# Kernel tuning notes

Hardware: AMD Instinct MI355X
Metric: run time of the kernel (lower is better)

## Reference

```python
import jax, jax.numpy as jnp
import numpy as np

N, J, H, O, SD = 6144, 2000, 100, 6144, 2


def setup_inputs() -> dict:
    key = jax.random.key(0)
    ks = jax.random.split(key, 18)
    sc = lambda fan_in: 1.0 / np.sqrt(fan_in)
    inp = {
        "gene_expr": jax.random.normal(ks[0], (N, J), jnp.float32),
        "spatial_pos": jax.random.normal(ks[1], (N, SD), jnp.float32),
        # linear weights stored [in, out] (y = x @ W + b)
        "Wq": jax.random.normal(ks[2], (J, H), jnp.float32) * sc(J),
        "bq": jnp.zeros((H,), jnp.float32),
        "Wk": jax.random.normal(ks[3], (J, H), jnp.float32) * sc(J),
        "bk": jnp.zeros((H,), jnp.float32),
        "Wv": jax.random.normal(ks[4], (J, O), jnp.float32) * sc(J),
        "bv": jnp.zeros((O,), jnp.float32),
        "Ws": jax.random.normal(ks[5], (SD, H), jnp.float32) * sc(SD),
        "bs": jnp.zeros((H,), jnp.float32),
        "W1": jax.random.normal(ks[6], (H, H), jnp.float32) * sc(H),
        "b1": jnp.zeros((H,), jnp.float32),
        "W2": jax.random.normal(ks[7], (H, H), jnp.float32) * sc(H),
        "b2": jnp.zeros((H,), jnp.float32),
        "Wf": jax.random.normal(ks[8], (H, 1), jnp.float32) * sc(H),
        "bf": jnp.zeros((1,), jnp.float32),
    }
    return inp


def reference(gene_expr, spatial_pos, Wq, bq, Wk, bk, Wv, bv, Ws, bs,
              W1, b1, W2, b2, Wf, bf):
    dk = jnp.sqrt(jnp.asarray(H, gene_expr.dtype))

    Q = gene_expr @ Wq + bq            # [N,H]
    K = gene_expr @ Wk + bk            # [N,H]
    V = gene_expr @ Wv + bv            # [N,O]

    # advanced spatial scalar + pairwise tanh difference
    sp = spatial_pos @ Ws + bs                             # [N,H]
    enh = jax.nn.relu(jnp.tanh(sp @ W1 + b1) @ W2 + b2)    # [N,H]
    f = (enh @ Wf + bf)[:, 0]                              # [N]
    fdiff = jnp.tanh(f[:, None] - f[None, :])              # [N,N]

    # gaussian kernel of squared pairwise distances (cdist p=2, sigma=1)
    sq = jnp.sum(spatial_pos * spatial_pos, axis=1)
    d2 = jnp.maximum(sq[:, None] + sq[None, :] - 2.0 * (spatial_pos @ spatial_pos.T), 0.0)
    spatial_sim = jnp.exp(-d2 / 2.0)                       # [N,N]

    # row-wise cosine similarity of gene expression
    norm = jnp.linalg.norm(gene_expr, axis=1, keepdims=True)
    xn = gene_expr / jnp.maximum(norm, 1e-12)
    cos_sim = xn @ xn.T                                    # [N,N]

    logits = (Q @ K.T) / dk + spatial_sim + cos_sim + fdiff
    attn = jax.nn.softmax(logits, axis=-1)                 # stable softmax == max-subtract in src
    out = attn @ V                                         # [N,O]
    return attn, out
```

## Files before the change

### kernel.cpp

```cpp
#include <hip/hip_runtime.h>
#include <stdint.h>
#include <math.h>

#define NN 6144
#define JJ 2000
#define HH 100
#define KB 2176
#define XOFF 128
#define KQK 2048

typedef __bf16 bf16;
typedef __bf16 bf16x8 __attribute__((ext_vector_type(8)));
typedef float f32x4 __attribute__((ext_vector_type(4)));

__device__ __forceinline__ void load_lds16(const void* g, void* l) {
  __builtin_amdgcn_global_load_lds(
      (const __attribute__((address_space(1))) void*)(uintptr_t)g,
      (__attribute__((address_space(3))) void*)(uint32_t)(uintptr_t)l,
      16, 0, 0);
}

template <int MODE>
__global__ __launch_bounds__(256, 2) void gemm_bt(
    const bf16* __restrict__ A, const bf16* __restrict__ B,
    int lda, int ldb, int kdim,
    const float* __restrict__ p0, const float* __restrict__ p1,
    const float* __restrict__ p2,
    bf16* __restrict__ ob0, bf16* __restrict__ ob1,
    float* __restrict__ of0, float* __restrict__ rowsum)
{
  __shared__ alignas(16) bf16 As[128 * 64];
  __shared__ alignas(16) bf16 Bs[128 * 64];

  const int tid = threadIdx.x;
  const int lane = tid & 63;
  const int wv = tid >> 6;
  const int m0 = blockIdx.x * 128;
  const int n0 = blockIdx.y * 128;

  const int srow = lane >> 3;
  const int scol = ((lane & 7) ^ srow) * 8;
  const bf16* gA = A + (size_t)(m0 + wv * 32 + srow) * lda + scol;
  const bf16* gB = B + (size_t)(n0 + wv * 32 + srow) * ldb + scol;
  bf16* lA0 = &As[(wv * 32) * 64];
  bf16* lB0 = &Bs[(wv * 32) * 64];

  const int l15 = lane & 15;
  const int l4 = lane >> 4;
  const int s7 = l15 & 7;
  const int wm = (wv >> 1) * 64;
  const int wn = (wv & 1) * 64;
  const bf16* ra0 = &As[(wm + l15) * 64 + ((l4 ^ s7) * 8)];
  const bf16* ra1 = &As[(wm + l15) * 64 + (((l4 + 4) ^ s7) * 8)];
  const bf16* rb0 = &Bs[(wn + l15) * 64 + ((l4 ^ s7) * 8)];
  const bf16* rb1 = &Bs[(wn + l15) * 64 + (((l4 + 4) ^ s7) * 8)];

  f32x4 acc[4][4];
#pragma unroll
  for (int i = 0; i < 4; ++i)
#pragma unroll
    for (int j = 0; j < 4; ++j) acc[i][j] = {0.f, 0.f, 0.f, 0.f};

  const int kiters = kdim >> 6;
  for (int kt = 0; kt < kiters; ++kt) {
    __syncthreads();
#pragma unroll
    for (int it = 0; it < 4; ++it) {
      load_lds16(gA + (size_t)it * 8 * lda, lA0 + it * 512);
      load_lds16(gB + (size_t)it * 8 * ldb, lB0 + it * 512);
    }
    gA += 64;
    gB += 64;
    __syncthreads();
#pragma unroll
    for (int ks = 0; ks < 2; ++ks) {
      const bf16* ra = ks ? ra1 : ra0;
      const bf16* rb = ks ? rb1 : rb0;
      bf16x8 af[4], bb[4];
#pragma unroll
      for (int i = 0; i < 4; ++i)
        af[i] = *(const bf16x8*)(ra + i * 1024);
#pragma unroll
      for (int j = 0; j < 4; ++j)
        bb[j] = *(const bf16x8*)(rb + j * 1024);
#pragma unroll
      for (int i = 0; i < 4; ++i)
#pragma unroll
        for (int j = 0; j < 4; ++j)
          acc[i][j] = __builtin_amdgcn_mfma_f32_16x16x32_bf16(af[i], bb[j], acc[i][j], 0, 0, 0);
    }
  }

  const int row_base = m0 + wm + l4 * 4;
  const int col_base = n0 + wn + l15;

  if (MODE == 3) {
#pragma unroll
    for (int i = 0; i < 4; ++i) {
#pragma unroll
      for (int r = 0; r < 4; ++r) {
        int row = row_base + i * 16 + r;
        float nm = p0[row];
#pragma unroll
        for (int j = 0; j < 4; ++j) {
          int h = col_base + j * 16;
          float v = acc[i][j][r] * nm;
          if (h < HH) ob0[(size_t)row * KB + h] = (bf16)((v + p1[h]) * 0.1f);
          else if (h < 2 * HH) ob1[(size_t)row * KB + (h - HH)] = (bf16)(v + p2[h - HH]);
        }
      }
    }
  }
}

__device__ __forceinline__ void gemm192_core(
    const bf16* __restrict__ A, const bf16* __restrict__ B,
    int lda, int ldb, int kdim, int m0, int n0, f32x4 (&acc)[6][4])
{
  __shared__ alignas(16) bf16 As[2][192 * 64];
  __shared__ alignas(16) bf16 Bs[2][256 * 64];

  const int tid = threadIdx.x;
  const int lane = tid & 63;
  const int wv = tid >> 6;
  const int wm = wv >> 2;
  const int wn = wv & 3;
  const int l15 = lane & 15;
  const int l4 = lane >> 4;
  const int s7 = lane & 7;
  const int srow = lane >> 3;
  const int scol = ((lane & 7) ^ srow) * 8;

  const bf16* gA = A + (size_t)(m0 + wv * 8 + srow) * lda + scol;
  const bf16* gB = B + (size_t)(n0 + wv * 8 + srow) * ldb + scol;

  const int c0 = (l4 ^ s7) * 8;
  const int c1 = ((l4 + 4) ^ s7) * 8;

#pragma unroll
  for (int i = 0; i < 6; ++i)
#pragma unroll
    for (int j = 0; j < 4; ++j) acc[i][j] = {0.f, 0.f, 0.f, 0.f};

  const int kt = kdim >> 6;

#define STA(bufi, h, T)                                                        \
  load_lds16(gA + (size_t)((h) * 64) * lda + (size_t)(T) * 64,                 \
             &As[(bufi)][((h) * 64 + wv * 8) * 64])
#define STB(bufi, h, T)                                                        \
  load_lds16(gB + (size_t)((h) * 64) * ldb + (size_t)(T) * 64,                 \
             &Bs[(bufi)][((h) * 64 + wv * 8) * 64])

  STA(0, 0, 0); STA(0, 1, 0); STA(0, 2, 0);
  STB(0, 0, 0); STB(0, 1, 0); STB(0, 2, 0); STB(0, 3, 0);
  STB(1, 0, 1); STB(1, 1, 1); STB(1, 2, 1); STB(1, 3, 1);
  asm volatile("s_waitcnt vmcnt(4)" ::: "memory");
  __builtin_amdgcn_s_barrier();

  bf16x8 af[6][2], b0[2][2], b1[2][2];

  for (int t2 = 0; t2 < kt; t2 += 2) {
#pragma unroll
    for (int u = 0; u < 2; ++u) {
      const int T = t2 + u;
      const int buf = u, bufn = u ^ 1;
      const bf16* pA = &As[buf][(wm * 96 + l15) * 64];
      const bf16* pB = &Bs[buf][(wn * 64 + l15) * 64];

#pragma unroll
      for (int fm = 0; fm < 6; ++fm) {
        af[fm][0] = *(const bf16x8*)(pA + (fm * 16) * 64 + c0);
        af[fm][1] = *(const bf16x8*)(pA + (fm * 16) * 64 + c1);
      }
#pragma unroll
      for (int fn = 0; fn < 2; ++fn) {
        b0[fn][0] = *(const bf16x8*)(pB + (fn * 16) * 64 + c0);
        b0[fn][1] = *(const bf16x8*)(pB + (fn * 16) * 64 + c1);
        b1[fn][0] = *(const bf16x8*)(pB + ((32 + fn * 16) * 64) + c0);
        b1[fn][1] = *(const bf16x8*)(pB + ((32 + fn * 16) * 64) + c1);
      }
      if (T + 1 < kt) { STA(bufn, 0, T + 1); STA(bufn, 1, T + 1); STA(bufn, 2, T + 1); }
      __builtin_amdgcn_s_setprio(1);
#pragma unroll
      for (int ks = 0; ks < 2; ++ks)
#pragma unroll
        for (int fm = 0; fm < 6; ++fm)
#pragma unroll
          for (int fn = 0; fn < 2; ++fn)
            acc[fm][fn] = __builtin_amdgcn_mfma_f32_16x16x32_bf16(
                af[fm][ks], b0[fn][ks], acc[fm][fn], 0, 0, 0);
      __builtin_amdgcn_s_setprio(0);
      asm volatile("s_waitcnt lgkmcnt(0)" ::: "memory");
      __builtin_amdgcn_s_barrier();

      if (T + 2 < kt) { STB(buf, 0, T + 2); STB(buf, 1, T + 2);
                        STB(buf, 2, T + 2); STB(buf, 3, T + 2); }
      __builtin_amdgcn_s_setprio(1);
#pragma unroll
      for (int ks = 0; ks < 2; ++ks)
#pragma unroll
        for (int fm = 0; fm < 6; ++fm)
#pragma unroll
          for (int fn = 0; fn < 2; ++fn)
            acc[fm][2 + fn] = __builtin_amdgcn_mfma_f32_16x16x32_bf16(
                af[fm][ks], b1[fn][ks], acc[fm][2 + fn], 0, 0, 0);
      __builtin_amdgcn_s_setprio(0);
      if (T + 1 < kt) {
        if (T + 2 < kt) asm volatile("s_waitcnt vmcnt(4)" ::: "memory");
        else            asm volatile("s_waitcnt vmcnt(0)" ::: "memory");
      }
      __builtin_amdgcn_s_barrier();
    }
  }
#undef STA
#undef STB
}

__global__ __launch_bounds__(512, 2) void gemm256_lv(
    const bf16* __restrict__ Abig, const bf16* __restrict__ WvT,
    const bf16* __restrict__ Bbig,
    const float* __restrict__ sqv, const float* __restrict__ fv,
    const float* __restrict__ spos, const float* __restrict__ normv,
    const float* __restrict__ bv,
    bf16* __restrict__ P, bf16* __restrict__ Vt, float* __restrict__ rowsum)
{
  int lin = blockIdx.y * 32 + blockIdx.x;
  int swz = (lin & 7) * 96 + (lin >> 3);
  const int m0 = (swz & 31) * 192;
  const int n0 = (swz >> 5) * 256;
  const bool isl = (blockIdx.z == 0);

  f32x4 acc[6][4];
  gemm192_core(isl ? Abig : WvT, Bbig, KB, KB, KB, m0, n0, acc);

  const int tid = threadIdx.x;
  const int lane = tid & 63;
  const int wv = tid >> 6;
  const int wm = wv >> 2, wn = wv & 3;
  const int l15 = lane & 15, l4 = lane >> 4;
  const int row_base = m0 + wm * 96 + l4 * 4;
  const int col_base = n0 + wn * 64 + l15;

  if (isl) {
    float sqc[4], fc[4], pxc[4], pyc[4];
#pragma unroll
    for (int j = 0; j < 4; ++j) {
      int c = col_base + j * 16;
      sqc[j] = sqv[c];
      fc[j] = fv[c];
      pxc[j] = spos[2 * c];
      pyc[j] = spos[2 * c + 1];
    }
#pragma unroll
    for (int i = 0; i < 6; ++i) {
#pragma unroll
      for (int r = 0; r < 4; ++r) {
        int row = row_base + i * 16 + r;
        float sqr = sqv[row], fr = fv[row];
        float pxr = spos[2 * row], pyr = spos[2 * row + 1];
        float rs = 0.f;
#pragma unroll
        for (int j = 0; j < 4; ++j) {
          int c = col_base + j * 16;
          float d2 = fmaxf(sqr + sqc[j] - 2.f * (pxr * pxc[j] + pyr * pyc[j]), 0.f);
          float lg = acc[i][j][r] + __expf(-0.5f * d2) + tanhf(fr - fc[j]);
          float e = __expf(lg);
          P[(size_t)row * NN + c] = (bf16)e;
          rs += e;
        }
        rs += __shfl_xor(rs, 1);
        rs += __shfl_xor(rs, 2);
        rs += __shfl_xor(rs, 4);
        rs += __shfl_xor(rs, 8);
        if (l15 == 0) atomicAdd(&rowsum[row], rs);
      }
    }
  } else {
    float nc[4];
#pragma unroll
    for (int j = 0; j < 4; ++j) nc[j] = normv[col_base + j * 16];
#pragma unroll
    for (int i = 0; i < 6; ++i) {
#pragma unroll
      for (int r = 0; r < 4; ++r) {
        int row = row_base + i * 16 + r;
        float bvr = bv[row];
#pragma unroll
        for (int j = 0; j < 4; ++j)
          Vt[(size_t)row * NN + col_base + j * 16] = (bf16)(acc[i][j][r] * nc[j] + bvr);
      }
    }
  }
}

__global__ __launch_bounds__(512, 2) void gemm256_pv(
    const bf16* __restrict__ Pm, const bf16* __restrict__ Vt,
    const float* __restrict__ rowsum, float* __restrict__ outp)
{
  int lin = blockIdx.y * 32 + blockIdx.x;
  int swz = (lin & 7) * 96 + (lin >> 3);
  const int m0 = (swz & 31) * 192;
  const int n0 = (swz >> 5) * 256;

  f32x4 acc[6][4];
  gemm192_core(Pm, Vt, NN, NN, NN, m0, n0, acc);

  const int tid = threadIdx.x;
  const int lane = tid & 63;
  const int wv = tid >> 6;
  const int wm = wv >> 2, wn = wv & 3;
  const int l15 = lane & 15, l4 = lane >> 4;
  const int row_base = m0 + wm * 96 + l4 * 4;
  const int col_base = n0 + wn * 64 + l15;
#pragma unroll
  for (int i = 0; i < 6; ++i) {
#pragma unroll
    for (int r = 0; r < 4; ++r) {
      int row = row_base + i * 16 + r;
      float rinv = 1.f / rowsum[row];
#pragma unroll
      for (int j = 0; j < 4; ++j)
        __builtin_nontemporal_store(acc[i][j][r] * rinv,
                                    &outp[(size_t)row * NN + col_base + j * 16]);
    }
  }
}

__global__ void prep_xn(const float* __restrict__ gene, bf16* __restrict__ Ab,
                        bf16* __restrict__ Bb, float* __restrict__ normv)
{
  int row = blockIdx.x, tid = threadIdx.x;
  const float* g = gene + (size_t)row * JJ;
  float s = 0.f;
  for (int k = tid; k < JJ; k += 256) { float v = g[k]; s += v * v; }
#pragma unroll
  for (int m = 32; m >= 1; m >>= 1) s += __shfl_xor(s, m);
  __shared__ float red[4];
  if ((tid & 63) == 0) red[tid >> 6] = s;
  __syncthreads();
  float tot = red[0] + red[1] + red[2] + red[3];
  float nrm = sqrtf(tot);
  float rinv = 1.f / fmaxf(nrm, 1e-12f);
  if (tid == 0) normv[row] = nrm;
  bf16* a = Ab + (size_t)row * KB;
  bf16* b = Bb + (size_t)row * KB;
  for (int k = tid; k < JJ; k += 256) {
    bf16 v = (bf16)(g[k] * rinv);
    a[XOFF + k] = v;
    b[XOFF + k] = v;
  }
  if (tid < 28) { a[HH + tid] = (bf16)0.f; b[HH + tid] = (bf16)0.f; }
  if (tid < 48) { a[XOFF + JJ + tid] = (bf16)0.f; b[XOFF + JJ + tid] = (bf16)0.f; }
}

__global__ void prep_sf(const float* __restrict__ spos,
                        const float* __restrict__ Ws, const float* __restrict__ bs,
                        const float* __restrict__ W1, const float* __restrict__ b1,
                        const float* __restrict__ W2, const float* __restrict__ b2,
                        const float* __restrict__ Wf, const float* __restrict__ bfp,
                        float* __restrict__ sqv, float* __restrict__ fv)
{
  int row = blockIdx.x, tid = threadIdx.x;
  float px = spos[2 * row], py = spos[2 * row + 1];
  if (tid == 0) sqv[row] = px * px + py * py;
  __shared__ float sp[HH], t1[HH], e2[HH];
  if (tid < HH) sp[tid] = px * Ws[tid] + py * Ws[HH + tid] + bs[tid];
  __syncthreads();
  if (tid < HH) {
    float s = b1[tid];
    for (int gi = 0; gi < HH; ++gi) s += sp[gi] * W1[gi * HH + tid];
    t1[tid] = tanhf(s);
  }
  __syncthreads();
  if (tid < HH) {
    float s = b2[tid];
    for (int gi = 0; gi < HH; ++gi) s += t1[gi] * W2[gi * HH + tid];
    e2[tid] = fmaxf(s, 0.f) * Wf[tid];
  }
  __syncthreads();
  if (tid < 64) {
    float s = e2[tid] + ((tid < 36) ? e2[tid + 64] : 0.f);
#pragma unroll
    for (int m = 32; m >= 1; m >>= 1) s += __shfl_xor(s, m);
    if (tid == 0) fv[row] = s + bfp[0];
  }
}

__global__ void pack_wqk(const float* __restrict__ Wq, const float* __restrict__ Wk,
                         bf16* __restrict__ Wt)
{
  int idx = blockIdx.x * 256 + threadIdx.x;
  int h = idx >> 11;
  int k = idx & 2047;
  float v = 0.f;
  if (k < JJ) {
    if (h < HH) v = Wq[(size_t)k * HH + h];
    else if (h < 2 * HH) v = Wk[(size_t)k * HH + (h - HH)];
  }
  Wt[idx] = (bf16)v;
}

__global__ void pack_wvt(const float* __restrict__ Wv, bf16* __restrict__ Wt)
{
  __shared__ float tile[32][33];
  int tx = threadIdx.x & 31, ty = threadIdx.x >> 5;
  int o0 = blockIdx.x * 32, j0 = blockIdx.y * 32;
#pragma unroll
  for (int rr = 0; rr < 32; rr += 8) {
    int j = j0 + ty + rr;
    tile[ty + rr][tx] = (j < JJ) ? Wv[(size_t)j * NN + o0 + tx] : 0.f;
  }
  __syncthreads();
#pragma unroll
  for (int rr = 0; rr < 32; rr += 8) {
    int o = o0 + ty + rr;
    Wt[(size_t)o * KB + XOFF + j0 + tx] = (bf16)tile[tx][ty + rr];
  }
}

__global__ void zero_wvt_head(bf16* __restrict__ Wt)
{
  int idx = blockIdx.x * 256 + threadIdx.x;
  int o = idx >> 7, c = idx & 127;
  Wt[(size_t)o * KB + c] = (bf16)0.f;
}

__global__ void norm_attn(const bf16* __restrict__ P, const float* __restrict__ rowsum,
                          float* __restrict__ attn)
{
  int row = blockIdx.x;
  float rinv = 1.f / rowsum[row];
  const bf16x8* p = (const bf16x8*)(P + (size_t)row * NN);
  float* dst = attn + (size_t)row * NN;
  for (int c = threadIdx.x; c < NN / 8; c += 256) {
    bf16x8 v = p[c];
#pragma unroll
    for (int e = 0; e < 8; ++e)
      __builtin_nontemporal_store((float)v[e] * rinv, &dst[c * 8 + e]);
  }
}

extern "C" void kernel_launch(void* const* d_in, const int* in_sizes, int n_in,
                              void* d_out, int out_size, void* d_ws, size_t ws_size,
                              hipStream_t stream)
{
  const float* gene = (const float*)d_in[0];
  const float* spos = (const float*)d_in[1];
  const float* Wq = (const float*)d_in[2];
  const float* bq = (const float*)d_in[3];
  const float* Wk = (const float*)d_in[4];
  const float* bk = (const float*)d_in[5];
  const float* Wv = (const float*)d_in[6];
  const float* bv = (const float*)d_in[7];
  const float* Ws = (const float*)d_in[8];
  const float* bs = (const float*)d_in[9];
  const float* W1 = (const float*)d_in[10];
  const float* b1 = (const float*)d_in[11];
  const float* W2 = (const float*)d_in[12];
  const float* b2 = (const float*)d_in[13];
  const float* Wf = (const float*)d_in[14];
  const float* bfp = (const float*)d_in[15];

  char* ws = (char*)d_ws;
  bf16* Abig = (bf16*)ws;            ws += (size_t)NN * KB * 2;
  bf16* Bbig = (bf16*)ws;            ws += (size_t)NN * KB * 2;
  bf16* WvT  = (bf16*)ws;            ws += (size_t)NN * KB * 2;
  bf16* WqkT = (bf16*)ws;            ws += (size_t)256 * KQK * 2;
  bf16* P    = (bf16*)ws;            ws += (size_t)NN * NN * 2;
  float* rowsum = (float*)ws;        ws += (size_t)NN * 4;
  float* normv  = (float*)ws;        ws += (size_t)NN * 4;
  float* sqv    = (float*)ws;        ws += (size_t)NN * 4;
  float* fv     = (float*)ws;        ws += (size_t)NN * 4;

  float* attn = (float*)d_out;
  float* outp = (float*)d_out + (size_t)NN * NN;
  bf16* Vt = (bf16*)d_out;

  hipMemsetAsync(rowsum, 0, NN * sizeof(float), stream);
  prep_xn<<<NN, 256, 0, stream>>>(gene, Abig, Bbig, normv);
  prep_sf<<<NN, 128, 0, stream>>>(spos, Ws, bs, W1, b1, W2, b2, Wf, bfp, sqv, fv);
  pack_wqk<<<(256 * KQK) / 256, 256, 0, stream>>>(Wq, Wk, WqkT);
  pack_wvt<<<dim3(NN / 32, KQK / 32), 256, 0, stream>>>(Wv, WvT);
  zero_wvt_head<<<(NN * XOFF) / 256, 256, 0, stream>>>(WvT);

  gemm_bt<3><<<dim3(NN / 128, 2), 256, 0, stream>>>(
      Abig + XOFF, WqkT, KB, KQK, KQK, normv, bq, bk, Abig, Bbig, nullptr, nullptr);
  gemm256_lv<<<dim3(32, 24, 2), 512, 0, stream>>>(
      Abig, WvT, Bbig, sqv, fv, spos, normv, bv, P, Vt, rowsum);
  gemm256_pv<<<dim3(32, 24), 512, 0, stream>>>(P, Vt, rowsum, outp);
  norm_attn<<<NN, 256, 0, stream>>>(P, rowsum, attn);
}
```

Measured before the change: 1.188 ms.

## Simplify GEMM pipeline, interleave L/V blocks, vectorize prep kernels, batch prep_sf rows

Replaces the staggered A/B double-buffer pipeline in the 192-row GEMM core with a simpler schedule that prefetches the whole next tile and syncs once per step. Interleaves logit and V-projection blocks in the grid and skips the zero head of WvT by starting its K range at the offset, which removes the zeroing kernel. Vectorizes prep_xn and norm_attn loads and stores, batches 8 rows per block in prep_sf, and replaces tanhf with an exp-based approximation. The simpler pipeline may lose the overlap of global loads with MFMA work.

```diff
diff --git a/kernel.cpp b/kernel.cpp
--- a/kernel.cpp
+++ b/kernel.cpp
@@ -18,6 +18,12 @@
       (const __attribute__((address_space(1))) void*)(uintptr_t)g,
       (__attribute__((address_space(3))) void*)(uint32_t)(uintptr_t)l,
       16, 0, 0);
+}
+
+__device__ __forceinline__ float ftanh(float x) {
+  float xc = fminf(fmaxf(x, -15.f), 15.f);
+  float e = __expf(2.f * xc);
+  return (e - 1.f) / (e + 1.f);
 }
 
 template <int MODE>
@@ -153,63 +159,40 @@
 
   STA(0, 0, 0); STA(0, 1, 0); STA(0, 2, 0);
   STB(0, 0, 0); STB(0, 1, 0); STB(0, 2, 0); STB(0, 3, 0);
-  STB(1, 0, 1); STB(1, 1, 1); STB(1, 2, 1); STB(1, 3, 1);
-  asm volatile("s_waitcnt vmcnt(4)" ::: "memory");
-  __builtin_amdgcn_s_barrier();
-
-  bf16x8 af[6][2], b0[2][2], b1[2][2];
+  __syncthreads();
 
   for (int t2 = 0; t2 < kt; t2 += 2) {
 #pragma unroll
     for (int u = 0; u < 2; ++u) {
       const int T = t2 + u;
-      const int buf = u, bufn = u ^ 1;
+      const int buf = u;
+      if (T + 1 < kt) {
+        STA(u ^ 1, 0, T + 1); STA(u ^ 1, 1, T + 1); STA(u ^ 1, 2, T + 1);
+        STB(u ^ 1, 0, T + 1); STB(u ^ 1, 1, T + 1);
+        STB(u ^ 1, 2, T + 1); STB(u ^ 1, 3, T + 1);
+      }
       const bf16* pA = &As[buf][(wm * 96 + l15) * 64];
       const bf16* pB = &Bs[buf][(wn * 64 + l15) * 64];
-
+      bf16x8 af[6][2], bb[4][2];
 #pragma unroll
       for (int fm = 0; fm < 6; ++fm) {
         af[fm][0] = *(const bf16x8*)(pA + (fm * 16) * 64 + c0);
         af[fm][1] = *(const bf16x8*)(pA + (fm * 16) * 64 + c1);
       }
 #pragma unroll
-      for (int fn = 0; fn < 2; ++fn) {
-        b0[fn][0] = *(const bf16x8*)(pB + (fn * 16) * 64 + c0);
-        b0[fn][1] = *(const bf16x8*)(pB + (fn * 16) * 64 + c1);
-        b1[fn][0] = *(const bf16x8*)(pB + ((32 + fn * 16) * 64) + c0);
-        b1[fn][1] = *(const bf16x8*)(pB + ((32 + fn * 16) * 64) + c1);
+      for (int fn = 0; fn < 4; ++fn) {
+        bb[fn][0] = *(const bf16x8*)(pB + (fn * 16) * 64 + c0);
+        bb[fn][1] = *(const bf16x8*)(pB + (fn * 16) * 64 + c1);
       }
-      if (T + 1 < kt) { STA(bufn, 0, T + 1); STA(bufn, 1, T + 1); STA(bufn, 2, T + 1); }
-      __builtin_amdgcn_s_setprio(1);
 #pragma unroll
       for (int ks = 0; ks < 2; ++ks)
 #pragma unroll
         for (int fm = 0; fm < 6; ++fm)
 #pragma unroll
-          for (int fn = 0; fn < 2; ++fn)
+          for (int fn = 0; fn < 4; ++fn)
             acc[fm][fn] = __builtin_amdgcn_mfma_f32_16x16x32_bf16(
-                af[fm][ks], b0[fn][ks], acc[fm][fn], 0, 0, 0);
-      __builtin_amdgcn_s_setprio(0);
-      asm volatile("s_waitcnt lgkmcnt(0)" ::: "memory");
-      __builtin_amdgcn_s_barrier();
-
-      if (T + 2 < kt) { STB(buf, 0, T + 2); STB(buf, 1, T + 2);
-                        STB(buf, 2, T + 2); STB(buf, 3, T + 2); }
-      __builtin_amdgcn_s_setprio(1);
-#pragma unroll
-      for (int ks = 0; ks < 2; ++ks)
-#pragma unroll
-        for (int fm = 0; fm < 6; ++fm)
-#pragma unroll
-          for (int fn = 0; fn < 2; ++fn)
-            acc[fm][2 + fn] = __builtin_amdgcn_mfma_f32_16x16x32_bf16(
-                af[fm][ks], b1[fn][ks], acc[fm][2 + fn], 0, 0, 0);
-      __builtin_amdgcn_s_setprio(0);
-      if (T + 1 < kt) {
-        if (T + 2 < kt) asm volatile("s_waitcnt vmcnt(4)" ::: "memory");
-        else            asm volatile("s_waitcnt vmcnt(0)" ::: "memory");
-      }
-      __builtin_amdgcn_s_barrier();
+                af[fm][ks], bb[fn][ks], acc[fm][fn], 0, 0, 0);
+      __syncthreads();
     }
   }
 #undef STA
@@ -224,14 +207,18 @@
     const float* __restrict__ bv,
     bf16* __restrict__ P, bf16* __restrict__ Vt, float* __restrict__ rowsum)
 {
-  int lin = blockIdx.y * 32 + blockIdx.x;
-  int swz = (lin & 7) * 96 + (lin >> 3);
+  int gid = (blockIdx.z * 24 + blockIdx.y) * 32 + blockIdx.x;
+  const bool isl = ((gid >> 3) & 1) == 0;
+  int work = (gid & 7) | ((gid >> 4) << 3);
+  int swz = (work & 7) * 96 + (work >> 3);
   const int m0 = (swz & 31) * 192;
   const int n0 = (swz >> 5) * 256;
-  const bool isl = (blockIdx.z == 0);
 
   f32x4 acc[6][4];
-  gemm192_core(isl ? Abig : WvT, Bbig, KB, KB, KB, m0, n0, acc);
+  if (isl)
+    gemm192_core(Abig, Bbig, KB, KB, KB, m0, n0, acc);
+  else
+    gemm192_core(WvT + XOFF, Bbig + XOFF, KB, KB, KQK, m0, n0, acc);
 
   const int tid = threadIdx.x;
   const int lane = tid & 63;
@@ -263,7 +250,7 @@
         for (int j = 0; j < 4; ++j) {
           int c = col_base + j * 16;
           float d2 = fmaxf(sqr + sqc[j] - 2.f * (pxr * pxc[j] + pyr * pyc[j]), 0.f);
-          float lg = acc[i][j][r] + __expf(-0.5f * d2) + tanhf(fr - fc[j]);
+          float lg = acc[i][j][r] + __expf(-0.5f * d2) + ftanh(fr - fc[j]);
           float e = __expf(lg);
           P[(size_t)row * NN + c] = (bf16)e;
           rs += e;
@@ -330,9 +317,12 @@
                         bf16* __restrict__ Bb, float* __restrict__ normv)
 {
   int row = blockIdx.x, tid = threadIdx.x;
-  const float* g = gene + (size_t)row * JJ;
+  const f32x4* g4 = (const f32x4*)(gene + (size_t)row * JJ);
   float s = 0.f;
-  for (int k = tid; k < JJ; k += 256) { float v = g[k]; s += v * v; }
+  for (int k = tid; k < 500; k += 256) {
+    f32x4 v = g4[k];
+    s += v[0] * v[0] + v[1] * v[1] + v[2] * v[2] + v[3] * v[3];
+  }
 #pragma unroll
   for (int m = 32; m >= 1; m >>= 1) s += __shfl_xor(s, m);
   __shared__ float red[4];
@@ -342,17 +332,25 @@
   float nrm = sqrtf(tot);
   float rinv = 1.f / fmaxf(nrm, 1e-12f);
   if (tid == 0) normv[row] = nrm;
-  bf16* a = Ab + (size_t)row * KB;
-  bf16* b = Bb + (size_t)row * KB;
-  for (int k = tid; k < JJ; k += 256) {
-    bf16 v = (bf16)(g[k] * rinv);
-    a[XOFF + k] = v;
-    b[XOFF + k] = v;
-  }
-  if (tid < 28) { a[HH + tid] = (bf16)0.f; b[HH + tid] = (bf16)0.f; }
-  if (tid < 48) { a[XOFF + JJ + tid] = (bf16)0.f; b[XOFF + JJ + tid] = (bf16)0.f; }
-}
-
+  bf16* a = Ab + (size_t)row * KB + XOFF;
+  bf16* b = Bb + (size_t)row * KB + XOFF;
+  for (int k = tid; k < 250; k += 256) {
+    f32x4 v0 = g4[2 * k], v1 = g4[2 * k + 1];
+    bf16x8 o;
+    o[0] = (bf16)(v0[0] * rinv); o[1] = (bf16)(v0[1] * rinv);
+    o[2] = (bf16)(v0[2] * rinv); o[3] = (bf16)(v0[3] * rinv);
+    o[4] = (bf16)(v1[0] * rinv); o[5] = (bf16)(v1[1] * rinv);
+    o[6] = (bf16)(v1[2] * rinv); o[7] = (bf16)(v1[3] * rinv);
+    *(bf16x8*)(a + k * 8) = o;
+    *(bf16x8*)(b + k * 8) = o;
+  }
+  bf16* a0 = Ab + (size_t)row * KB;
+  bf16* b0 = Bb + (size_t)row * KB;
+  if (tid < 28) { a0[HH + tid] = (bf16)0.f; b0[HH + tid] = (bf16)0.f; }
+  if (tid < 48) { a0[XOFF + JJ + tid] = (bf16)0.f; b0[XOFF + JJ + tid] = (bf16)0.f; }
+}
+
+#define SFR 8
 __global__ void prep_sf(const float* __restrict__ spos,
                         const float* __restrict__ Ws, const float* __restrict__ bs,
                         const float* __restrict__ W1, const float* __restrict__ b1,
@@ -360,30 +358,56 @@
                         const float* __restrict__ Wf, const float* __restrict__ bfp,
                         float* __restrict__ sqv, float* __restrict__ fv)
 {
-  int row = blockIdx.x, tid = threadIdx.x;
-  float px = spos[2 * row], py = spos[2 * row + 1];
-  if (tid == 0) sqv[row] = px * px + py * py;
-  __shared__ float sp[HH], t1[HH], e2[HH];
-  if (tid < HH) sp[tid] = px * Ws[tid] + py * Ws[HH + tid] + bs[tid];
+  int row0 = blockIdx.x * SFR, tid = threadIdx.x;
+  __shared__ float sp[SFR][HH], t1[SFR][HH], e2[SFR][HH];
+  float px[SFR], py[SFR];
+#pragma unroll
+  for (int r = 0; r < SFR; ++r) {
+    px[r] = spos[2 * (row0 + r)];
+    py[r] = spos[2 * (row0 + r) + 1];
+  }
+  if (tid < SFR) sqv[row0 + tid] = px[tid] * px[tid] + py[tid] * py[tid];
+  if (tid < HH) {
+    float w0 = Ws[tid], w1 = Ws[HH + tid], bsv = bs[tid];
+#pragma unroll
+    for (int r = 0; r < SFR; ++r) sp[r][tid] = px[r] * w0 + py[r] * w1 + bsv;
+  }
   __syncthreads();
   if (tid < HH) {
-    float s = b1[tid];
-    for (int gi = 0; gi < HH; ++gi) s += sp[gi] * W1[gi * HH + tid];
-    t1[tid] = tanhf(s);
+    float s[SFR];
+#pragma unroll
+    for (int r = 0; r < SFR; ++r) s[r] = b1[tid];
+    for (int gi = 0; gi < HH; ++gi) {
+      float w = W1[gi * HH + tid];
+#pragma unroll
+      for (int r = 0; r < SFR; ++r) s[r] += sp[r][gi] * w;
+    }
+#pragma unroll
+    for (int r = 0; r < SFR; ++r) t1[r][tid] = ftanh(s[r]);
   }
   __syncthreads();
   if (tid < HH) {
-    float s = b2[tid];
-    for (int gi = 0; gi < HH; ++gi) s += t1[gi] * W2[gi * HH + tid];
-    e2[tid] = fmaxf(s, 0.f) * Wf[tid];
+    float s[SFR];
+#pragma unroll
+    for (int r = 0; r < SFR; ++r) s[r] = b2[tid];
+    for (int gi = 0; gi < HH; ++gi) {
+      float w = W2[gi * HH + tid];
+#pragma unroll
+      for (int r = 0; r < SFR; ++r) s[r] += t1[r][gi] * w;
+    }
+    float wf = Wf[tid];
+#pragma unroll
+    for (int r = 0; r < SFR; ++r) e2[r][tid] = fmaxf(s[r], 0.f) * wf;
   }
   __syncthreads();
-  if (tid < 64) {
-    float s = e2[tid] + ((tid < 36) ? e2[tid + 64] : 0.f);
-#pragma unroll
-    for (int m = 32; m >= 1; m >>= 1) s += __shfl_xor(s, m);
-    if (tid == 0) fv[row] = s + bfp[0];
-  }
+  int g = tid >> 4, l = tid & 15;
+  float s = 0.f;
+  for (int k = l; k < HH; k += 16) s += e2[g][k];
+  s += __shfl_xor(s, 1);
+  s += __shfl_xor(s, 2);
+  s += __shfl_xor(s, 4);
+  s += __shfl_xor(s, 8);
+  if (l == 0) fv[row0 + g] = s + bfp[0];
 }
 
 __global__ void pack_wqk(const float* __restrict__ Wq, const float* __restrict__ Wk,
@@ -418,25 +442,21 @@
   }
 }
 
-__global__ void zero_wvt_head(bf16* __restrict__ Wt)
-{
-  int idx = blockIdx.x * 256 + threadIdx.x;
-  int o = idx >> 7, c = idx & 127;
-  Wt[(size_t)o * KB + c] = (bf16)0.f;
-}
-
 __global__ void norm_attn(const bf16* __restrict__ P, const float* __restrict__ rowsum,
                           float* __restrict__ attn)
 {
   int row = blockIdx.x;
   float rinv = 1.f / rowsum[row];
   const bf16x8* p = (const bf16x8*)(P + (size_t)row * NN);
-  float* dst = attn + (size_t)row * NN;
+  f32x4* dst = (f32x4*)(attn + (size_t)row * NN);
   for (int c = threadIdx.x; c < NN / 8; c += 256) {
     bf16x8 v = p[c];
-#pragma unroll
-    for (int e = 0; e < 8; ++e)
-      __builtin_nontemporal_store((float)v[e] * rinv, &dst[c * 8 + e]);
+    f32x4 o0 = {(float)v[0] * rinv, (float)v[1] * rinv,
+                (float)v[2] * rinv, (float)v[3] * rinv};
+    f32x4 o1 = {(float)v[4] * rinv, (float)v[5] * rinv,
+                (float)v[6] * rinv, (float)v[7] * rinv};
+    __builtin_nontemporal_store(o0, &dst[2 * c]);
+    __builtin_nontemporal_store(o1, &dst[2 * c + 1]);
   }
 }
 
@@ -478,10 +498,9 @@
 
   hipMemsetAsync(rowsum, 0, NN * sizeof(float), stream);
   prep_xn<<<NN, 256, 0, stream>>>(gene, Abig, Bbig, normv);
-  prep_sf<<<NN, 128, 0, stream>>>(spos, Ws, bs, W1, b1, W2, b2, Wf, bfp, sqv, fv);
+  prep_sf<<<NN / SFR, 128, 0, stream>>>(spos, Ws, bs, W1, b1, W2, b2, Wf, bfp, sqv, fv);
   pack_wqk<<<(256 * KQK) / 256, 256, 0, stream>>>(Wq, Wk, WqkT);
   pack_wvt<<<dim3(NN / 32, KQK / 32), 256, 0, stream>>>(Wv, WvT);
-  zero_wvt_head<<<(NN * XOFF) / 256, 256, 0, stream>>>(WvT);
 
   gemm_bt<3><<<dim3(NN / 128, 2), 256, 0, stream>>>(
       Abig + XOFF, WqkT, KB, KQK, KQK, normv, bq, bk, Abig, Bbig, nullptr, nullptr);
```

New measurement: 1.240 ms. 1.04x slower.
